# Kernel optimization log

Hardware: AMD Instinct MI355X
Metric: run time of the kernel (lower is better)

The kernel has to match this reference:

```python
import jax, jax.numpy as jnp
import numpy as np
from jax import lax

T = 1.0      # terminal time
SIGMA = 1.0  # diffusion coefficient
N, D, P, M, H = 16384, 16, 8, 50, 128


def setup_inputs() -> dict:
    key = jax.random.key(0)
    ks = jax.random.split(key, 8)
    scale1 = 1.0 / np.sqrt(1 + D + P)
    scale2 = 1.0 / np.sqrt(H)
    return {
        "initial_states": jax.random.normal(ks[0], (N, D), jnp.float32),
        "initial_values": jax.random.normal(ks[1], (N,), jnp.float32),
        "observations": jax.random.normal(ks[2], (N, P), jnp.float32),
        "noise": jax.random.normal(ks[3], (M, N, D), jnp.float32),
        "W1": jax.random.normal(ks[4], (1 + D + P, H), jnp.float32) * scale1,
        "b1": jnp.zeros((H,), jnp.float32),
        "W2": jax.random.normal(ks[5], (H, H), jnp.float32) * scale2,
        "b2": jnp.zeros((H,), jnp.float32),
        "W3": jax.random.normal(ks[6], (H, D), jnp.float32) * scale2,
        "b3": jnp.zeros((D,), jnp.float32),
    }


def reference(initial_states, initial_values, observations, noise,
              W1, b1, W2, b2, W3, b3):
    """Euler-Maruyama rollout of simulate_SDEs: joint (X, V) SDE with
    per-step Z-network drift. drift b(X) = -X (OU process)."""
    m_steps = noise.shape[0]
    dt = jnp.asarray(T / m_steps, initial_states.dtype)
    sqrt_dt = jnp.sqrt(dt)
    times = jnp.arange(m_steps, dtype=initial_states.dtype) * dt  # time[m]

    def z_net(t, X, Y):
        tcol = jnp.full((X.shape[0], 1), t, X.dtype)
        h = jnp.concatenate([tcol, X, Y], axis=1)      # (N, 1+d+p)
        h = jax.nn.relu(h @ W1 + b1)
        h = jax.nn.relu(h @ W2 + b2)
        return h @ W3 + b3                             # (N, d)

    def step(carry, inp):
        X, V = carry
        eps, t = inp
        Wn = sqrt_dt * eps                             # Brownian increment
        Z = z_net(t, X, observations)
        drift_V = 0.5 * jnp.sum(Z * Z, axis=1)
        V = V + dt * drift_V + jnp.sum(Z * Wn, axis=1)
        X = X + dt * (-X) + SIGMA * Wn                 # b(X) = -X
        return (X, V), None

    (X, V), _ = lax.scan(step, (initial_states, initial_values), (noise, times))
    return X, V
```

## Files before the change

### kernel.cpp

```cpp
#include <hip/hip_runtime.h>

typedef __bf16   bf16x8 __attribute__((ext_vector_type(8)));
typedef float    f32x4  __attribute__((ext_vector_type(4)));
typedef float    f32x2  __attribute__((ext_vector_type(2)));
typedef uint32_t u32x4  __attribute__((ext_vector_type(4)));

constexpr int N_ = 16384;
constexpr int D_ = 16;
constexpr int P_ = 8;
constexpr int H_ = 128;
constexpr int M_ = 50;

__device__ __forceinline__ uint32_t pk_bf16(float a, float b) {
    uint32_t ua = __builtin_bit_cast(uint32_t, a) + 0x8000u;
    uint32_t ub = __builtin_bit_cast(uint32_t, b) + 0x8000u;
    return __builtin_amdgcn_perm(ub, ua, 0x07060302u);
}
__device__ __forceinline__ uint32_t pk_relu_bf16(float a, float b) {
    return pk_bf16(fmaxf(a, 0.0f), fmaxf(b, 0.0f));
}

__global__ __launch_bounds__(64, 1)
void sde_fused(const float* __restrict__ X0,
               const float* __restrict__ V0,
               const float* __restrict__ Yobs,
               const float* __restrict__ noise,
               const float* __restrict__ W1, const float* __restrict__ b1,
               const float* __restrict__ W2, const float* __restrict__ b2,
               const float* __restrict__ W3, const float* __restrict__ b3,
               float* __restrict__ out)
{
    const int lane = threadIdx.x;
    const int n    = lane & 15;
    const int q    = lane >> 4;
    const int gr   = blockIdx.x * 16 + n;

    const float dt   = 0.02f;
    const float sqdt = 0.1414213562373095f;

    bf16x8 w1f[8];
#pragma unroll
    for (int ct = 0; ct < 8; ++ct) {
        u32x4 u;
        u[0] = pk_bf16(W1[(1 + q * 4 + 0) * H_ + ct * 16 + n],
                       W1[(1 + q * 4 + 1) * H_ + ct * 16 + n]);
        u[1] = pk_bf16(W1[(1 + q * 4 + 2) * H_ + ct * 16 + n],
                       W1[(1 + q * 4 + 3) * H_ + ct * 16 + n]);
        u[2] = pk_bf16(W1[(17 + q * 2 + 0) * H_ + ct * 16 + n],
                       W1[(17 + q * 2 + 1) * H_ + ct * 16 + n]);
        u[3] = (q == 0) ? pk_bf16(b1[ct * 16 + n], W1[ct * 16 + n]) : 0u;
        w1f[ct] = __builtin_bit_cast(bf16x8, u);
    }
    bf16x8 w2f[8][4];
#pragma unroll
    for (int ct = 0; ct < 8; ++ct)
#pragma unroll
        for (int kt = 0; kt < 4; ++kt) {
            u32x4 u;
#pragma unroll
            for (int w = 0; w < 4; ++w) {
                int h0 = (kt * 2 + (w >> 1)) * 16 + q * 4 + (w & 1) * 2;
                u[w] = pk_bf16(W2[h0 * H_ + ct * 16 + n],
                               W2[(h0 + 1) * H_ + ct * 16 + n]);
            }
            w2f[ct][kt] = __builtin_bit_cast(bf16x8, u);
        }
    bf16x8 w3f[4];
#pragma unroll
    for (int kt = 0; kt < 4; ++kt) {
        u32x4 u;
#pragma unroll
        for (int w = 0; w < 4; ++w) {
            int h0 = (kt * 2 + (w >> 1)) * 16 + q * 4 + (w & 1) * 2;
            u[w] = pk_bf16(W3[h0 * D_ + n], W3[(h0 + 1) * D_ + n]);
        }
        w3f[kt] = __builtin_bit_cast(bf16x8, u);
    }
    f32x4 b2r[8];
#pragma unroll
    for (int ct = 0; ct < 8; ++ct)
#pragma unroll
        for (int r = 0; r < 4; ++r) b2r[ct][r] = b2[ct * 16 + q * 4 + r];
    f32x4 b3r;
#pragma unroll
    for (int r = 0; r < 4; ++r) b3r[r] = b3[q * 4 + r];

    f32x4 x = *(const f32x4*)&X0[gr * D_ + q * 4];
    f32x2 y2 = *(const f32x2*)&Yobs[gr * P_ + q * 2];
    const uint32_t yw = pk_bf16(y2[0], y2[1]);

    const float* npb = noise + (size_t)gr * D_ + q * 4;
    f32x4 e0 = *(const f32x4*)npb;
    f32x4 e1 = *(const f32x4*)(npb + (size_t)N_ * D_);
    float t = 0.0f;
    float vacc = 0.0f;

    for (int m = 0; m < M_; ++m) {
        int mp = (m + 2 < M_) ? (m + 2) : (M_ - 1);
        f32x4 e2 = *(const f32x4*)(npb + (size_t)mp * N_ * D_);

        u32x4 au;
        au[0] = pk_bf16(x[0], x[1]);
        au[1] = pk_bf16(x[2], x[3]);
        au[2] = yw;
        au[3] = (q == 0) ? pk_bf16(1.0f, t) : 0u;
        bf16x8 a0 = __builtin_bit_cast(bf16x8, au);

        f32x4 h1c[8];
#pragma unroll
        for (int ct = 0; ct < 8; ++ct)
            h1c[ct] = __builtin_amdgcn_mfma_f32_16x16x32_bf16(
                w1f[ct], a0, (f32x4){0.f, 0.f, 0.f, 0.f}, 0, 0, 0);

        bf16x8 h1b[4];
#pragma unroll
        for (int kt = 0; kt < 4; ++kt) {
            u32x4 u;
            u[0] = pk_relu_bf16(h1c[2 * kt][0], h1c[2 * kt][1]);
            u[1] = pk_relu_bf16(h1c[2 * kt][2], h1c[2 * kt][3]);
            u[2] = pk_relu_bf16(h1c[2 * kt + 1][0], h1c[2 * kt + 1][1]);
            u[3] = pk_relu_bf16(h1c[2 * kt + 1][2], h1c[2 * kt + 1][3]);
            h1b[kt] = __builtin_bit_cast(bf16x8, u);
        }

        f32x4 h2c[8];
#pragma unroll
        for (int ct = 0; ct < 8; ++ct) {
            f32x4 c = b2r[ct];
#pragma unroll
            for (int kt = 0; kt < 4; ++kt)
                c = __builtin_amdgcn_mfma_f32_16x16x32_bf16(w2f[ct][kt], h1b[kt], c, 0, 0, 0);
            h2c[ct] = c;
        }
        bf16x8 h2b[4];
#pragma unroll
        for (int kt = 0; kt < 4; ++kt) {
            u32x4 u;
            u[0] = pk_relu_bf16(h2c[2 * kt][0], h2c[2 * kt][1]);
            u[1] = pk_relu_bf16(h2c[2 * kt][2], h2c[2 * kt][3]);
            u[2] = pk_relu_bf16(h2c[2 * kt + 1][0], h2c[2 * kt + 1][1]);
            u[3] = pk_relu_bf16(h2c[2 * kt + 1][2], h2c[2 * kt + 1][3]);
            h2b[kt] = __builtin_bit_cast(bf16x8, u);
        }

        f32x4 za = __builtin_amdgcn_mfma_f32_16x16x32_bf16(w3f[0], h2b[0], b3r, 0, 0, 0);
        za = __builtin_amdgcn_mfma_f32_16x16x32_bf16(w3f[1], h2b[1], za, 0, 0, 0);
        f32x4 zb = __builtin_amdgcn_mfma_f32_16x16x32_bf16(
            w3f[2], h2b[2], (f32x4){0.f, 0.f, 0.f, 0.f}, 0, 0, 0);
        zb = __builtin_amdgcn_mfma_f32_16x16x32_bf16(w3f[3], h2b[3], zb, 0, 0, 0);

#pragma unroll
        for (int r = 0; r < 4; ++r) {
            float z  = za[r] + zb[r];
            float wn = sqdt * e0[r];
            vacc = fmaf(z, wn, fmaf(0.01f * z, z, vacc));
            x[r] = fmaf(x[r], 0.98f, wn);
        }

        e0 = e1; e1 = e2;
        t += dt;
    }

    float part = vacc;
    part += __shfl_xor(part, 16);
    part += __shfl_xor(part, 32);
    float v = V0[gr] + part;

    *(f32x4*)&out[gr * D_ + q * 4] = x;
    if (q == 0) out[N_ * D_ + gr] = v;
}

extern "C" void kernel_launch(void* const* d_in, const int* in_sizes, int n_in,
                              void* d_out, int out_size, void* d_ws, size_t ws_size,
                              hipStream_t stream)
{
    const float* X0 = (const float*)d_in[0];
    const float* V0 = (const float*)d_in[1];
    const float* Y  = (const float*)d_in[2];
    const float* nz = (const float*)d_in[3];
    const float* W1 = (const float*)d_in[4];
    const float* b1 = (const float*)d_in[5];
    const float* W2 = (const float*)d_in[6];
    const float* b2 = (const float*)d_in[7];
    const float* W3 = (const float*)d_in[8];
    const float* b3 = (const float*)d_in[9];
    float* out = (float*)d_out;

    sde_fused<<<N_ / 16, 64, 0, stream>>>(X0, V0, Y, nz, W1, b1, W2, b2, W3, b3, out);
}
```

Baseline: 138.1 us.

## Split hidden dimension across two waves per block with LDS exchange

Each 16-row block now runs two wavefronts. Each wave owns half of the hidden columns of W1/W2 and half of the K-tiles of W3, so per-wave MFMA work and weight-register footprint are halved. Partial h1 activations and partial Z outputs are exchanged through shared memory with two __syncthreads per time step. The intent is to shorten the serial per-step dependency chain and raise occupancy. The cost is barrier and LDS traffic on every step, plus duplicated X/V update work in both waves.

```diff
diff --git a/kernel.cpp b/kernel.cpp
--- a/kernel.cpp
+++ b/kernel.cpp
@@ -20,7 +20,7 @@
     return pk_bf16(fmaxf(a, 0.0f), fmaxf(b, 0.0f));
 }
 
-__global__ __launch_bounds__(64, 1)
+__global__ __launch_bounds__(128, 2)
 void sde_fused(const float* __restrict__ X0,
                const float* __restrict__ V0,
                const float* __restrict__ Yobs,
@@ -30,7 +30,12 @@
                const float* __restrict__ W3, const float* __restrict__ b3,
                float* __restrict__ out)
 {
-    const int lane = threadIdx.x;
+    __shared__ u32x4 ex1[4][64];
+    __shared__ f32x4 ex2[2][64];
+
+    const int tid  = threadIdx.x;
+    const int wv   = tid >> 6;
+    const int lane = tid & 63;
     const int n    = lane & 15;
     const int q    = lane >> 4;
     const int gr   = blockIdx.x * 16 + n;
@@ -38,9 +43,10 @@
     const float dt   = 0.02f;
     const float sqdt = 0.1414213562373095f;
 
-    bf16x8 w1f[8];
-#pragma unroll
-    for (int ct = 0; ct < 8; ++ct) {
+    bf16x8 w1f[4];
+#pragma unroll
+    for (int c = 0; c < 4; ++c) {
+        int ct = wv * 4 + c;
         u32x4 u;
         u[0] = pk_bf16(W1[(1 + q * 4 + 0) * H_ + ct * 16 + n],
                        W1[(1 + q * 4 + 1) * H_ + ct * 16 + n]);
@@ -49,11 +55,12 @@
         u[2] = pk_bf16(W1[(17 + q * 2 + 0) * H_ + ct * 16 + n],
                        W1[(17 + q * 2 + 1) * H_ + ct * 16 + n]);
         u[3] = (q == 0) ? pk_bf16(b1[ct * 16 + n], W1[ct * 16 + n]) : 0u;
-        w1f[ct] = __builtin_bit_cast(bf16x8, u);
-    }
-    bf16x8 w2f[8][4];
-#pragma unroll
-    for (int ct = 0; ct < 8; ++ct)
+        w1f[c] = __builtin_bit_cast(bf16x8, u);
+    }
+    bf16x8 w2f[4][4];
+#pragma unroll
+    for (int c = 0; c < 4; ++c) {
+        int ct = wv * 4 + c;
 #pragma unroll
         for (int kt = 0; kt < 4; ++kt) {
             u32x4 u;
@@ -63,27 +70,29 @@
                 u[w] = pk_bf16(W2[h0 * H_ + ct * 16 + n],
                                W2[(h0 + 1) * H_ + ct * 16 + n]);
             }
-            w2f[ct][kt] = __builtin_bit_cast(bf16x8, u);
-        }
-    bf16x8 w3f[4];
-#pragma unroll
-    for (int kt = 0; kt < 4; ++kt) {
+            w2f[c][kt] = __builtin_bit_cast(bf16x8, u);
+        }
+    }
+    bf16x8 w3f[2];
+#pragma unroll
+    for (int i = 0; i < 2; ++i) {
+        int kt = wv * 2 + i;
         u32x4 u;
 #pragma unroll
         for (int w = 0; w < 4; ++w) {
             int h0 = (kt * 2 + (w >> 1)) * 16 + q * 4 + (w & 1) * 2;
             u[w] = pk_bf16(W3[h0 * D_ + n], W3[(h0 + 1) * D_ + n]);
         }
-        w3f[kt] = __builtin_bit_cast(bf16x8, u);
-    }
-    f32x4 b2r[8];
-#pragma unroll
-    for (int ct = 0; ct < 8; ++ct)
-#pragma unroll
-        for (int r = 0; r < 4; ++r) b2r[ct][r] = b2[ct * 16 + q * 4 + r];
-    f32x4 b3r;
-#pragma unroll
-    for (int r = 0; r < 4; ++r) b3r[r] = b3[q * 4 + r];
+        w3f[i] = __builtin_bit_cast(bf16x8, u);
+    }
+    f32x4 b2r[4];
+#pragma unroll
+    for (int c = 0; c < 4; ++c)
+#pragma unroll
+        for (int r = 0; r < 4; ++r) b2r[c][r] = b2[(wv * 4 + c) * 16 + q * 4 + r];
+    f32x4 zinit;
+#pragma unroll
+    for (int r = 0; r < 4; ++r) zinit[r] = (wv == 0) ? b3[q * 4 + r] : 0.0f;
 
     f32x4 x = *(const f32x4*)&X0[gr * D_ + q * 4];
     f32x2 y2 = *(const f32x2*)&Yobs[gr * P_ + q * 2];
@@ -106,52 +115,67 @@
         au[3] = (q == 0) ? pk_bf16(1.0f, t) : 0u;
         bf16x8 a0 = __builtin_bit_cast(bf16x8, au);
 
-        f32x4 h1c[8];
-#pragma unroll
-        for (int ct = 0; ct < 8; ++ct)
-            h1c[ct] = __builtin_amdgcn_mfma_f32_16x16x32_bf16(
-                w1f[ct], a0, (f32x4){0.f, 0.f, 0.f, 0.f}, 0, 0, 0);
+        f32x4 h1c[4];
+#pragma unroll
+        for (int c = 0; c < 4; ++c)
+            h1c[c] = __builtin_amdgcn_mfma_f32_16x16x32_bf16(
+                w1f[c], a0, (f32x4){0.f, 0.f, 0.f, 0.f}, 0, 0, 0);
+
+        u32x4 p0, p1;
+        p0[0] = pk_relu_bf16(h1c[0][0], h1c[0][1]);
+        p0[1] = pk_relu_bf16(h1c[0][2], h1c[0][3]);
+        p0[2] = pk_relu_bf16(h1c[1][0], h1c[1][1]);
+        p0[3] = pk_relu_bf16(h1c[1][2], h1c[1][3]);
+        p1[0] = pk_relu_bf16(h1c[2][0], h1c[2][1]);
+        p1[1] = pk_relu_bf16(h1c[2][2], h1c[2][3]);
+        p1[2] = pk_relu_bf16(h1c[3][0], h1c[3][1]);
+        p1[3] = pk_relu_bf16(h1c[3][2], h1c[3][3]);
+
+        ex1[2 * wv + 0][lane] = p0;
+        ex1[2 * wv + 1][lane] = p1;
+        __syncthreads();
 
         bf16x8 h1b[4];
-#pragma unroll
-        for (int kt = 0; kt < 4; ++kt) {
-            u32x4 u;
-            u[0] = pk_relu_bf16(h1c[2 * kt][0], h1c[2 * kt][1]);
-            u[1] = pk_relu_bf16(h1c[2 * kt][2], h1c[2 * kt][3]);
-            u[2] = pk_relu_bf16(h1c[2 * kt + 1][0], h1c[2 * kt + 1][1]);
-            u[3] = pk_relu_bf16(h1c[2 * kt + 1][2], h1c[2 * kt + 1][3]);
-            h1b[kt] = __builtin_bit_cast(bf16x8, u);
-        }
-
-        f32x4 h2c[8];
-#pragma unroll
-        for (int ct = 0; ct < 8; ++ct) {
-            f32x4 c = b2r[ct];
+        h1b[2 * wv + 0] = __builtin_bit_cast(bf16x8, p0);
+        h1b[2 * wv + 1] = __builtin_bit_cast(bf16x8, p1);
+        {
+            int o = 2 - 2 * wv;
+            h1b[o + 0] = __builtin_bit_cast(bf16x8, ex1[o + 0][lane]);
+            h1b[o + 1] = __builtin_bit_cast(bf16x8, ex1[o + 1][lane]);
+        }
+
+        f32x4 h2c[4];
+#pragma unroll
+        for (int c = 0; c < 4; ++c) {
+            f32x4 cc = b2r[c];
 #pragma unroll
             for (int kt = 0; kt < 4; ++kt)
-                c = __builtin_amdgcn_mfma_f32_16x16x32_bf16(w2f[ct][kt], h1b[kt], c, 0, 0, 0);
-            h2c[ct] = c;
-        }
-        bf16x8 h2b[4];
-#pragma unroll
-        for (int kt = 0; kt < 4; ++kt) {
-            u32x4 u;
-            u[0] = pk_relu_bf16(h2c[2 * kt][0], h2c[2 * kt][1]);
-            u[1] = pk_relu_bf16(h2c[2 * kt][2], h2c[2 * kt][3]);
-            u[2] = pk_relu_bf16(h2c[2 * kt + 1][0], h2c[2 * kt + 1][1]);
-            u[3] = pk_relu_bf16(h2c[2 * kt + 1][2], h2c[2 * kt + 1][3]);
-            h2b[kt] = __builtin_bit_cast(bf16x8, u);
-        }
-
-        f32x4 za = __builtin_amdgcn_mfma_f32_16x16x32_bf16(w3f[0], h2b[0], b3r, 0, 0, 0);
-        za = __builtin_amdgcn_mfma_f32_16x16x32_bf16(w3f[1], h2b[1], za, 0, 0, 0);
-        f32x4 zb = __builtin_amdgcn_mfma_f32_16x16x32_bf16(
-            w3f[2], h2b[2], (f32x4){0.f, 0.f, 0.f, 0.f}, 0, 0, 0);
-        zb = __builtin_amdgcn_mfma_f32_16x16x32_bf16(w3f[3], h2b[3], zb, 0, 0, 0);
+                cc = __builtin_amdgcn_mfma_f32_16x16x32_bf16(w2f[c][kt], h1b[kt], cc, 0, 0, 0);
+            h2c[c] = cc;
+        }
+
+        u32x4 q0, q1;
+        q0[0] = pk_relu_bf16(h2c[0][0], h2c[0][1]);
+        q0[1] = pk_relu_bf16(h2c[0][2], h2c[0][3]);
+        q0[2] = pk_relu_bf16(h2c[1][0], h2c[1][1]);
+        q0[3] = pk_relu_bf16(h2c[1][2], h2c[1][3]);
+        q1[0] = pk_relu_bf16(h2c[2][0], h2c[2][1]);
+        q1[1] = pk_relu_bf16(h2c[2][2], h2c[2][3]);
+        q1[2] = pk_relu_bf16(h2c[3][0], h2c[3][1]);
+        q1[3] = pk_relu_bf16(h2c[3][2], h2c[3][3]);
+
+        f32x4 zp = __builtin_amdgcn_mfma_f32_16x16x32_bf16(
+            w3f[0], __builtin_bit_cast(bf16x8, q0), zinit, 0, 0, 0);
+        zp = __builtin_amdgcn_mfma_f32_16x16x32_bf16(
+            w3f[1], __builtin_bit_cast(bf16x8, q1), zp, 0, 0, 0);
+
+        ex2[wv][lane] = zp;
+        __syncthreads();
+        f32x4 zo = ex2[1 - wv][lane];
 
 #pragma unroll
         for (int r = 0; r < 4; ++r) {
-            float z  = za[r] + zb[r];
+            float z  = zp[r] + zo[r];
             float wn = sqdt * e0[r];
             vacc = fmaf(z, wn, fmaf(0.01f * z, z, vacc));
             x[r] = fmaf(x[r], 0.98f, wn);
@@ -166,8 +190,10 @@
     part += __shfl_xor(part, 32);
     float v = V0[gr] + part;
 
-    *(f32x4*)&out[gr * D_ + q * 4] = x;
-    if (q == 0) out[N_ * D_ + gr] = v;
+    if (wv == 0) {
+        *(f32x4*)&out[gr * D_ + q * 4] = x;
+        if (q == 0) out[N_ * D_ + gr] = v;
+    }
 }
 
 extern "C" void kernel_launch(void* const* d_in, const int* in_sizes, int n_in,
@@ -186,5 +212,5 @@
     const float* b3 = (const float*)d_in[9];
     float* out = (float*)d_out;
 
-    sde_fused<<<N_ / 16, 64, 0, stream>>>(X0, V0, Y, nz, W1, b1, W2, b2, W3, b3, out);
-}
+    sde_fused<<<N_ / 16, 128, 0, stream>>>(X0, V0, Y, nz, W1, b1, W2, b2, W3, b3, out);
+}
```

New measurement: 523.8 us. 3.79x slower.

## Process two SDE steps per iteration to interleave independent MLP evaluations

Applied to the files above, without the earlier changes.

The X update never depends on the network output Z, so the states for two consecutive time steps can be computed up front. The two Z-network evaluations then run as independent MFMA chains that the compiler can interleave, hiding MFMA and dependency latency in a wave that runs alone on its SIMD. Noise prefetch is also deepened from two steps ahead to four. The cost is roughly doubled live intermediate registers, which raises the risk of spills. Time values are now accumulated in 0.04 increments, which changes rounding slightly.

```diff
diff --git a/kernel.cpp b/kernel.cpp
--- a/kernel.cpp
+++ b/kernel.cpp
@@ -90,28 +90,20 @@
     const uint32_t yw = pk_bf16(y2[0], y2[1]);
 
     const float* npb = noise + (size_t)gr * D_ + q * 4;
-    f32x4 e0 = *(const f32x4*)npb;
-    f32x4 e1 = *(const f32x4*)(npb + (size_t)N_ * D_);
-    float t = 0.0f;
+    const size_t stp = (size_t)N_ * D_;
+    f32x4 e0 = *(const f32x4*)(npb + 0 * stp);
+    f32x4 e1 = *(const f32x4*)(npb + 1 * stp);
+    f32x4 e2 = *(const f32x4*)(npb + 2 * stp);
+    f32x4 e3 = *(const f32x4*)(npb + 3 * stp);
+    float tA = 0.0f, tB = dt;
     float vacc = 0.0f;
 
-    for (int m = 0; m < M_; ++m) {
-        int mp = (m + 2 < M_) ? (m + 2) : (M_ - 1);
-        f32x4 e2 = *(const f32x4*)(npb + (size_t)mp * N_ * D_);
-
-        u32x4 au;
-        au[0] = pk_bf16(x[0], x[1]);
-        au[1] = pk_bf16(x[2], x[3]);
-        au[2] = yw;
-        au[3] = (q == 0) ? pk_bf16(1.0f, t) : 0u;
-        bf16x8 a0 = __builtin_bit_cast(bf16x8, au);
-
+    auto mlp = [&](bf16x8 a0) -> f32x4 {
         f32x4 h1c[8];
 #pragma unroll
         for (int ct = 0; ct < 8; ++ct)
             h1c[ct] = __builtin_amdgcn_mfma_f32_16x16x32_bf16(
                 w1f[ct], a0, (f32x4){0.f, 0.f, 0.f, 0.f}, 0, 0, 0);
-
         bf16x8 h1b[4];
 #pragma unroll
         for (int kt = 0; kt < 4; ++kt) {
@@ -122,15 +114,14 @@
             u[3] = pk_relu_bf16(h1c[2 * kt + 1][2], h1c[2 * kt + 1][3]);
             h1b[kt] = __builtin_bit_cast(bf16x8, u);
         }
-
         f32x4 h2c[8];
 #pragma unroll
         for (int ct = 0; ct < 8; ++ct) {
-            f32x4 c = b2r[ct];
+            f32x4 cc = b2r[ct];
 #pragma unroll
             for (int kt = 0; kt < 4; ++kt)
-                c = __builtin_amdgcn_mfma_f32_16x16x32_bf16(w2f[ct][kt], h1b[kt], c, 0, 0, 0);
-            h2c[ct] = c;
+                cc = __builtin_amdgcn_mfma_f32_16x16x32_bf16(w2f[ct][kt], h1b[kt], cc, 0, 0, 0);
+            h2c[ct] = cc;
         }
         bf16x8 h2b[4];
 #pragma unroll
@@ -142,23 +133,57 @@
             u[3] = pk_relu_bf16(h2c[2 * kt + 1][2], h2c[2 * kt + 1][3]);
             h2b[kt] = __builtin_bit_cast(bf16x8, u);
         }
-
         f32x4 za = __builtin_amdgcn_mfma_f32_16x16x32_bf16(w3f[0], h2b[0], b3r, 0, 0, 0);
         za = __builtin_amdgcn_mfma_f32_16x16x32_bf16(w3f[1], h2b[1], za, 0, 0, 0);
         f32x4 zb = __builtin_amdgcn_mfma_f32_16x16x32_bf16(
             w3f[2], h2b[2], (f32x4){0.f, 0.f, 0.f, 0.f}, 0, 0, 0);
         zb = __builtin_amdgcn_mfma_f32_16x16x32_bf16(w3f[3], h2b[3], zb, 0, 0, 0);
-
+        f32x4 zr;
+#pragma unroll
+        for (int r = 0; r < 4; ++r) zr[r] = za[r] + zb[r];
+        return zr;
+    };
+
+    for (int mm = 0; mm < M_ / 2; ++mm) {
+        int sa = 2 * mm + 4; if (sa > M_ - 1) sa = M_ - 1;
+        int sb = 2 * mm + 5; if (sb > M_ - 1) sb = M_ - 1;
+        f32x4 e4 = *(const f32x4*)(npb + (size_t)sa * stp);
+        f32x4 e5 = *(const f32x4*)(npb + (size_t)sb * stp);
+
+        u32x4 auA;
+        auA[0] = pk_bf16(x[0], x[1]);
+        auA[1] = pk_bf16(x[2], x[3]);
+        auA[2] = yw;
+        auA[3] = (q == 0) ? pk_bf16(1.0f, tA) : 0u;
+        f32x4 wnA, xB, wnB;
 #pragma unroll
         for (int r = 0; r < 4; ++r) {
-            float z  = za[r] + zb[r];
-            float wn = sqdt * e0[r];
-            vacc = fmaf(z, wn, fmaf(0.01f * z, z, vacc));
-            x[r] = fmaf(x[r], 0.98f, wn);
-        }
-
-        e0 = e1; e1 = e2;
-        t += dt;
+            wnA[r] = sqdt * e0[r];
+            xB[r]  = fmaf(x[r], 0.98f, wnA[r]);
+        }
+        u32x4 auB;
+        auB[0] = pk_bf16(xB[0], xB[1]);
+        auB[1] = pk_bf16(xB[2], xB[3]);
+        auB[2] = yw;
+        auB[3] = (q == 0) ? pk_bf16(1.0f, tB) : 0u;
+#pragma unroll
+        for (int r = 0; r < 4; ++r) {
+            wnB[r] = sqdt * e1[r];
+            x[r]   = fmaf(xB[r], 0.98f, wnB[r]);
+        }
+
+        f32x4 zA = mlp(__builtin_bit_cast(bf16x8, auA));
+        f32x4 zB = mlp(__builtin_bit_cast(bf16x8, auB));
+
+#pragma unroll
+        for (int r = 0; r < 4; ++r)
+            vacc = fmaf(zA[r], wnA[r], fmaf(0.01f * zA[r], zA[r], vacc));
+#pragma unroll
+        for (int r = 0; r < 4; ++r)
+            vacc = fmaf(zB[r], wnB[r], fmaf(0.01f * zB[r], zB[r], vacc));
+
+        e0 = e2; e1 = e3; e2 = e4; e3 = e5;
+        tA += 0.04f; tB += 0.04f;
     }
 
     float part = vacc;
```

After: 139.1 us. No clear change (+0.7%).

## Split the time loop across two waves and stage W2 weights in LDS

Applied to the files above, without the earlier changes.

The X recurrence does not depend on the Z network, so a second wave first advances X through the first 25 steps with the cheap OU update. The two waves then each evaluate the MLP drift for half of the 50 steps, and their V partial sums are combined through shared memory. This halves the serial dependency chain per row and doubles the number of waves. W2 fragments move from registers into LDS so that two waves per block fit in the register budget, at the cost of LDS reads on every step and a redundant pass over half of the noise.

```diff
diff --git a/kernel.cpp b/kernel.cpp
--- a/kernel.cpp
+++ b/kernel.cpp
@@ -20,7 +20,7 @@
     return pk_bf16(fmaxf(a, 0.0f), fmaxf(b, 0.0f));
 }
 
-__global__ __launch_bounds__(64, 1)
+__global__ __launch_bounds__(128, 2)
 void sde_fused(const float* __restrict__ X0,
                const float* __restrict__ V0,
                const float* __restrict__ Yobs,
@@ -30,13 +30,32 @@
                const float* __restrict__ W3, const float* __restrict__ b3,
                float* __restrict__ out)
 {
-    const int lane = threadIdx.x;
+    __shared__ u32x4 w2lds[8][4][64];
+    __shared__ float vsh[2][16];
+
+    const int tid  = threadIdx.x;
+    const int wv   = tid >> 6;
+    const int lane = tid & 63;
     const int n    = lane & 15;
     const int q    = lane >> 4;
     const int gr   = blockIdx.x * 16 + n;
 
     const float dt   = 0.02f;
     const float sqdt = 0.1414213562373095f;
+
+#pragma unroll
+    for (int i = 0; i < 16; ++i) {
+        int idx = wv * 16 + i;
+        int ct = idx >> 2, kt = idx & 3;
+        u32x4 u;
+#pragma unroll
+        for (int w = 0; w < 4; ++w) {
+            int h0 = (kt * 2 + (w >> 1)) * 16 + q * 4 + (w & 1) * 2;
+            u[w] = pk_bf16(W2[h0 * H_ + ct * 16 + n],
+                           W2[(h0 + 1) * H_ + ct * 16 + n]);
+        }
+        w2lds[ct][kt][lane] = u;
+    }
 
     bf16x8 w1f[8];
 #pragma unroll
@@ -51,20 +70,6 @@
         u[3] = (q == 0) ? pk_bf16(b1[ct * 16 + n], W1[ct * 16 + n]) : 0u;
         w1f[ct] = __builtin_bit_cast(bf16x8, u);
     }
-    bf16x8 w2f[8][4];
-#pragma unroll
-    for (int ct = 0; ct < 8; ++ct)
-#pragma unroll
-        for (int kt = 0; kt < 4; ++kt) {
-            u32x4 u;
-#pragma unroll
-            for (int w = 0; w < 4; ++w) {
-                int h0 = (kt * 2 + (w >> 1)) * 16 + q * 4 + (w & 1) * 2;
-                u[w] = pk_bf16(W2[h0 * H_ + ct * 16 + n],
-                               W2[(h0 + 1) * H_ + ct * 16 + n]);
-            }
-            w2f[ct][kt] = __builtin_bit_cast(bf16x8, u);
-        }
     bf16x8 w3f[4];
 #pragma unroll
     for (int kt = 0; kt < 4; ++kt) {
@@ -90,14 +95,29 @@
     const uint32_t yw = pk_bf16(y2[0], y2[1]);
 
     const float* npb = noise + (size_t)gr * D_ + q * 4;
-    f32x4 e0 = *(const f32x4*)npb;
-    f32x4 e1 = *(const f32x4*)(npb + (size_t)N_ * D_);
-    float t = 0.0f;
+    const size_t stp = (size_t)N_ * D_;
+
+    if (wv == 1) {
+#pragma unroll 5
+        for (int m = 0; m < 25; ++m) {
+            f32x4 ee = *(const f32x4*)(npb + (size_t)m * stp);
+#pragma unroll
+            for (int r = 0; r < 4; ++r)
+                x[r] = fmaf(x[r], 0.98f, sqdt * ee[r]);
+        }
+    }
+
+    __syncthreads();
+
+    const float* base = npb + (size_t)(wv * 25) * stp;
+    f32x4 e0 = *(const f32x4*)(base);
+    f32x4 e1 = *(const f32x4*)(base + stp);
+    float t = wv ? 0.5f : 0.0f;
     float vacc = 0.0f;
 
-    for (int m = 0; m < M_; ++m) {
-        int mp = (m + 2 < M_) ? (m + 2) : (M_ - 1);
-        f32x4 e2 = *(const f32x4*)(npb + (size_t)mp * N_ * D_);
+    for (int m = 0; m < 25; ++m) {
+        int mp = (m + 2 < 25) ? (m + 2) : 24;
+        f32x4 e2 = *(const f32x4*)(base + (size_t)mp * stp);
 
         u32x4 au;
         au[0] = pk_bf16(x[0], x[1]);
@@ -126,12 +146,18 @@
         f32x4 h2c[8];
 #pragma unroll
         for (int ct = 0; ct < 8; ++ct) {
-            f32x4 c = b2r[ct];
-#pragma unroll
-            for (int kt = 0; kt < 4; ++kt)
-                c = __builtin_amdgcn_mfma_f32_16x16x32_bf16(w2f[ct][kt], h1b[kt], c, 0, 0, 0);
-            h2c[ct] = c;
-        }
+            bf16x8 f0 = __builtin_bit_cast(bf16x8, w2lds[ct][0][lane]);
+            bf16x8 f1 = __builtin_bit_cast(bf16x8, w2lds[ct][1][lane]);
+            bf16x8 f2 = __builtin_bit_cast(bf16x8, w2lds[ct][2][lane]);
+            bf16x8 f3 = __builtin_bit_cast(bf16x8, w2lds[ct][3][lane]);
+            f32x4 cc = b2r[ct];
+            cc = __builtin_amdgcn_mfma_f32_16x16x32_bf16(f0, h1b[0], cc, 0, 0, 0);
+            cc = __builtin_amdgcn_mfma_f32_16x16x32_bf16(f1, h1b[1], cc, 0, 0, 0);
+            cc = __builtin_amdgcn_mfma_f32_16x16x32_bf16(f2, h1b[2], cc, 0, 0, 0);
+            cc = __builtin_amdgcn_mfma_f32_16x16x32_bf16(f3, h1b[3], cc, 0, 0, 0);
+            h2c[ct] = cc;
+        }
+
         bf16x8 h2b[4];
 #pragma unroll
         for (int kt = 0; kt < 4; ++kt) {
@@ -164,10 +190,13 @@
     float part = vacc;
     part += __shfl_xor(part, 16);
     part += __shfl_xor(part, 32);
-    float v = V0[gr] + part;
-
-    *(f32x4*)&out[gr * D_ + q * 4] = x;
-    if (q == 0) out[N_ * D_ + gr] = v;
+    if (q == 0) vsh[wv][n] = part;
+    __syncthreads();
+
+    if (wv == 1) {
+        *(f32x4*)&out[gr * D_ + q * 4] = x;
+        if (q == 0) out[N_ * D_ + gr] = V0[gr] + vsh[0][n] + vsh[1][n];
+    }
 }
 
 extern "C" void kernel_launch(void* const* d_in, const int* in_sizes, int n_in,
@@ -186,5 +215,5 @@
     const float* b3 = (const float*)d_in[9];
     float* out = (float*)d_out;
 
-    sde_fused<<<N_ / 16, 64, 0, stream>>>(X0, V0, Y, nz, W1, b1, W2, b2, W3, b3, out);
-}
+    sde_fused<<<N_ / 16, 128, 0, stream>>>(X0, V0, Y, nz, W1, b1, W2, b2, W3, b3, out);
+}
```

Result: slower. 153.5 us (+11.2%).
